# Performance work log

Measured on AMD Instinct MI355X. Metric: run time of the kernel, lower is better.

Reference implementation:

```python
import jax, jax.numpy as jnp
import numpy as np

B, T, D, H = 2, 2048, 2048, 16
DH = D // H

def setup_inputs() -> dict:
    key = jax.random.key(0)
    k1, k2, k3 = jax.random.split(key, 3)
    x = jax.random.normal(k1, (B, T, D), dtype=jnp.float32)
    w_qkv = jax.random.normal(k2, (D, 3 * D), dtype=jnp.float32) * (1.0 / np.sqrt(D))
    w_o = jax.random.normal(k3, (D, D), dtype=jnp.float32) * (1.0 / np.sqrt(D))
    return {"x": x, "w_qkv": w_qkv, "w_o": w_o}

def reference(x, w_qkv, w_o):
    b, t, d = x.shape
    qkv = (x @ w_qkv).reshape(b, t, 3, H, DH)
    q, k, v = qkv[:, :, 0], qkv[:, :, 1], qkv[:, :, 2]  # [b,t,h,dh]
    scale = 1.0 / np.sqrt(DH).astype(np.float32)
    # scores: [b,h,t,t]
    scores = jnp.einsum('bqhd,bkhd->bhqk', q, k) * scale
    causal = jnp.tril(jnp.ones((t, t), dtype=bool))
    scores = jnp.where(causal[None, None], scores, -jnp.inf)
    attn = jax.nn.softmax(scores, axis=-1)
    out = jnp.einsum('bhqk,bkhd->bqhd', attn, v).reshape(b, t, d)
    return out @ w_o
```

## Files before the change

kernel.cpp:

```cpp
#include <hip/hip_runtime.h>
#include <hip/hip_bf16.h>

#define B_   2
#define T_   2048
#define D_   2048
#define H_   16
#define DH_  128
#define TD3_ 6144

typedef __attribute__((ext_vector_type(8))) short   short8;
typedef __attribute__((ext_vector_type(8))) unsigned short ushort8v;
typedef __attribute__((ext_vector_type(4))) float   f32x4;
typedef __attribute__((ext_vector_type(4))) float   f4v;
typedef __attribute__((ext_vector_type(4))) unsigned short u16x4;

static __device__ __forceinline__ unsigned short f2bf(float f) {
  unsigned int u = __builtin_bit_cast(unsigned int, f);
  u += 0x7FFFu + ((u >> 16) & 1u);
  return (unsigned short)(u >> 16);
}
static __device__ __forceinline__ float bf2f(unsigned short u) {
  return __builtin_bit_cast(float, (unsigned int)u << 16);
}

static __device__ __forceinline__ void gload_lds16(const unsigned short* g, unsigned short* l) {
  __builtin_amdgcn_global_load_lds((const __attribute__((address_space(1))) void*)g,
                                   (__attribute__((address_space(3))) void*)l, 16, 0, 0);
}

__global__ __launch_bounds__(256) void convert_f32_bf16(const float* __restrict__ X,
                                                        unsigned short* __restrict__ Y, int n4) {
  for (int i = blockIdx.x * blockDim.x + threadIdx.x; i < n4; i += gridDim.x * blockDim.x) {
    f4v v = ((const f4v*)X)[i];
    u16x4 o;
    o[0] = f2bf(v[0]); o[1] = f2bf(v[1]); o[2] = f2bf(v[2]); o[3] = f2bf(v[3]);
    ((u16x4*)Y)[i] = o;
  }
}

__global__ __launch_bounds__(256) void transpose_f32_bf16(const float* __restrict__ W,
                                                          unsigned short* __restrict__ WT,
                                                          int K, int N) {
  __shared__ float tile[32][33];
  int n0 = blockIdx.x * 32, k0 = blockIdx.y * 32;
  int tx = threadIdx.x & 31, ty = threadIdx.x >> 5;
#pragma unroll
  for (int r = 0; r < 4; r++)
    tile[ty + 8 * r][tx] = W[(size_t)(k0 + ty + 8 * r) * N + n0 + tx];
  __syncthreads();
#pragma unroll
  for (int r = 0; r < 4; r++)
    WT[(size_t)(n0 + ty + 8 * r) * K + k0 + tx] = f2bf(tile[tx][ty + 8 * r]);
}

__global__ __launch_bounds__(256) void vtr_kernel(const unsigned short* __restrict__ qkv,
                                                  unsigned short* __restrict__ vtg) {
  __shared__ unsigned short tile[64][68];
  const int t0 = blockIdx.x * 64;
  const int h = blockIdx.y >> 1, dh0 = (blockIdx.y & 1) * 64;
  const int b = blockIdx.z;
  const int tid = threadIdx.x;
  const unsigned short* src = qkv + (size_t)b * T_ * TD3_ + 2 * D_ + h * DH_ + dh0;
  {
    const int r = tid >> 3, cc = (tid & 7) * 8;
#pragma unroll
    for (int k = 0; k < 2; k++) {
      ushort8v v = *(const ushort8v*)(src + (size_t)(t0 + k * 32 + r) * TD3_ + cc);
      *(ushort8v*)&tile[k * 32 + r][cc] = v;
    }
  }
  __syncthreads();
  unsigned short* dst = vtg + ((size_t)(b * H_ + h) * DH_ + dh0) * T_ + t0;
  {
    const int d = tid >> 3, tc = (tid & 7) * 8;
#pragma unroll
    for (int k = 0; k < 2; k++) {
      ushort8v v;
#pragma unroll
      for (int j = 0; j < 8; j++) v[j] = tile[tc + j][k * 32 + d];
      *(ushort8v*)(dst + (size_t)(k * 32 + d) * T_ + tc) = v;
    }
  }
}

template <int OUTBF>
__global__ __launch_bounds__(512, 1) void gemm256(const unsigned short* __restrict__ A,
                                                  const unsigned short* __restrict__ BT,
                                                  void* __restrict__ C, int M, int N, int K) {
  __shared__ unsigned short lA[2][2][128 * 64];
  __shared__ unsigned short lB[2][2][128 * 64];

  const int tid = threadIdx.x;
  const int nwg = gridDim.x;
  const int swz = ((int)blockIdx.x & 7) * (nwg >> 3) + ((int)blockIdx.x >> 3);
  const int nbx = N >> 8;
  const int m0 = (swz / nbx) * 256, n0 = (swz % nbx) * 256;
  const int l = tid & 63, lr = l & 15, lg = l >> 4;
  const int wid = tid >> 6, wm = wid >> 2, wn = wid & 3;
  const int bh = wn >> 1, br0 = (wn & 1) * 64;
  const int nk = K >> 6;

  f32x4 acc[8][4] = {};

  auto stageA = [&](int buf, int h, int kt) {
#pragma unroll
    for (int q = 0; q < 2; q++) {
      const int n = q * 512 + tid;
      const int row = n >> 3, ch = n & 7;
      gload_lds16(A + (size_t)(m0 + h * 128 + row) * K + kt * 64 + ((ch ^ (row & 7)) << 3),
                  &lA[buf][h][n * 8]);
    }
  };
  auto stageB = [&](int buf, int h, int kt) {
#pragma unroll
    for (int q = 0; q < 2; q++) {
      const int n = q * 512 + tid;
      const int row = n >> 3, ch = n & 7;
      gload_lds16(BT + (size_t)(n0 + h * 128 + row) * K + kt * 64 + ((ch ^ (row & 7)) << 3),
                  &lB[buf][h][n * 8]);
    }
  };

  stageB(0, 0, 0); stageA(0, 0, 0); stageB(0, 1, 0); stageA(0, 1, 0);
  if (nk > 1) {
    stageB(1, 0, 1); stageA(1, 0, 1);
    asm volatile("s_waitcnt vmcnt(4)" ::: "memory");
  } else {
    asm volatile("s_waitcnt vmcnt(0)" ::: "memory");
  }
  __builtin_amdgcn_s_barrier();

  short8 a[4][2], b0[2][2], b1[2][2];
  for (int kt = 0; kt < nk; kt++) {
    const int buf = kt & 1;

#pragma unroll
    for (int mi = 0; mi < 4; mi++)
#pragma unroll
      for (int kk = 0; kk < 2; kk++) {
        const int row = mi * 16 + lr;
        a[mi][kk] = *(const short8*)&lA[buf][wm][row * 64 + (((kk * 4 + lg) ^ (lr & 7)) << 3)];
      }
#pragma unroll
    for (int ni = 0; ni < 2; ni++)
#pragma unroll
      for (int kk = 0; kk < 2; kk++) {
        const int row = br0 + ni * 16 + lr;
        b0[ni][kk] = *(const short8*)&lB[buf][bh][row * 64 + (((kk * 4 + lg) ^ (lr & 7)) << 3)];
      }
    if (kt + 1 < nk) stageB(buf ^ 1, 1, kt + 1);
    __builtin_amdgcn_s_barrier();
    __builtin_amdgcn_s_setprio(1);
#pragma unroll
    for (int mi = 0; mi < 4; mi++)
#pragma unroll
      for (int ni = 0; ni < 2; ni++)
#pragma unroll
        for (int kk = 0; kk < 2; kk++)
          acc[mi][ni] = __builtin_amdgcn_mfma_f32_16x16x32_bf16(a[mi][kk], b0[ni][kk], acc[mi][ni], 0, 0, 0);
    __builtin_amdgcn_s_setprio(0);
    __builtin_amdgcn_s_barrier();

#pragma unroll
    for (int ni = 0; ni < 2; ni++)
#pragma unroll
      for (int kk = 0; kk < 2; kk++) {
        const int row = br0 + (2 + ni) * 16 + lr;
        b1[ni][kk] = *(const short8*)&lB[buf][bh][row * 64 + (((kk * 4 + lg) ^ (lr & 7)) << 3)];
      }
    if (kt + 1 < nk) stageA(buf ^ 1, 1, kt + 1);
    __builtin_amdgcn_s_barrier();
    __builtin_amdgcn_s_setprio(1);
#pragma unroll
    for (int mi = 0; mi < 4; mi++)
#pragma unroll
      for (int ni = 0; ni < 2; ni++)
#pragma unroll
        for (int kk = 0; kk < 2; kk++)
          acc[mi][2 + ni] = __builtin_amdgcn_mfma_f32_16x16x32_bf16(a[mi][kk], b1[ni][kk], acc[mi][2 + ni], 0, 0, 0);
    __builtin_amdgcn_s_setprio(0);
    __builtin_amdgcn_s_barrier();

#pragma unroll
    for (int mi = 0; mi < 4; mi++)
#pragma unroll
      for (int kk = 0; kk < 2; kk++) {
        const int row = (4 + mi) * 16 + lr;
        a[mi][kk] = *(const short8*)&lA[buf][wm][row * 64 + (((kk * 4 + lg) ^ (lr & 7)) << 3)];
      }
    if (kt + 2 < nk) stageB(buf, 0, kt + 2);
    __builtin_amdgcn_s_barrier();
    __builtin_amdgcn_s_setprio(1);
#pragma unroll
    for (int mi = 0; mi < 4; mi++)
#pragma unroll
      for (int ni = 0; ni < 2; ni++)
#pragma unroll
        for (int kk = 0; kk < 2; kk++)
          acc[4 + mi][2 + ni] = __builtin_amdgcn_mfma_f32_16x16x32_bf16(a[mi][kk], b1[ni][kk], acc[4 + mi][2 + ni], 0, 0, 0);
    __builtin_amdgcn_s_setprio(0);
    __builtin_amdgcn_s_barrier();

    if (kt + 2 < nk) stageA(buf, 0, kt + 2);
    __builtin_amdgcn_s_barrier();
    __builtin_amdgcn_s_setprio(1);
#pragma unroll
    for (int mi = 0; mi < 4; mi++)
#pragma unroll
      for (int ni = 0; ni < 2; ni++)
#pragma unroll
        for (int kk = 0; kk < 2; kk++)
          acc[4 + mi][ni] = __builtin_amdgcn_mfma_f32_16x16x32_bf16(a[mi][kk], b0[ni][kk], acc[4 + mi][ni], 0, 0, 0);
    __builtin_amdgcn_s_setprio(0);
    if (kt + 2 < nk) asm volatile("s_waitcnt vmcnt(4)" ::: "memory");
    else             asm volatile("s_waitcnt vmcnt(0)" ::: "memory");
    __builtin_amdgcn_s_barrier();
  }

#pragma unroll
  for (int mi = 0; mi < 8; mi++)
#pragma unroll
    for (int ni = 0; ni < 4; ni++)
#pragma unroll
      for (int i = 0; i < 4; i++) {
        const int row = m0 + wm * 128 + mi * 16 + lg * 4 + i;
        const int col = n0 + wn * 64 + ni * 16 + lr;
        if (OUTBF) ((unsigned short*)C)[(size_t)row * N + col] = f2bf(acc[mi][ni][i]);
        else       ((float*)C)[(size_t)row * N + col] = acc[mi][ni][i];
      }
}

__global__ __launch_bounds__(256, 2) void attn_fa(const unsigned short* __restrict__ qkv,
                                                  const unsigned short* __restrict__ vtg,
                                                  unsigned short* __restrict__ out) {
  const int x = blockIdx.x, h = blockIdx.y, b = blockIdx.z;
  const int qtl = b ? x : (T_ / 128 - 1 - x);
  const int q0 = qtl * 128;
  const int tid = threadIdx.x, w = tid >> 6, l = tid & 63, lr = l & 15, lg = l >> 4;

  const unsigned short* Qb = qkv + (size_t)b * T_ * TD3_ + h * DH_;
  const unsigned short* Kb = Qb + D_;
  const unsigned short* Vt = vtg + ((size_t)b * H_ + h) * DH_ * T_;

  __shared__ unsigned short klds[2][64 * 128];
  __shared__ unsigned short vt[2][128 * 64];
  __shared__ unsigned short plds[4][32 * 64];

  const float scale = 0.08838834764831845f;

  short8 qf[2][4];
#pragma unroll
  for (int mi = 0; mi < 2; mi++) {
    const unsigned short* qrow = Qb + (size_t)(q0 + w * 32 + mi * 16 + lr) * TD3_;
#pragma unroll
    for (int ks = 0; ks < 4; ks++) {
      ushort8v qv = *(const ushort8v*)(qrow + ks * 32 + lg * 8);
      short8 qs;
#pragma unroll
      for (int j = 0; j < 8; j++) qs[j] = (short)f2bf(bf2f(qv[j]) * scale);
      qf[mi][ks] = qs;
    }
  }

  f32x4 oacc[2][8] = {};
  float mrun[2][4], lsum[2][4];
#pragma unroll
  for (int mi = 0; mi < 2; mi++)
#pragma unroll
    for (int i = 0; i < 4; i++) { mrun[mi][i] = -__builtin_inff(); lsum[mi][i] = 0.f; }

  auto STAGE = [&](int buf, int kv0) {
#pragma unroll
    for (int it = 0; it < 4; it++) {
      const int n = it * 256 + tid;
      { const int kv = n >> 4, ch = n & 15;
        gload_lds16(Kb + (size_t)(kv0 + kv) * TD3_ + ((ch ^ (kv & 7)) << 3),
                    &klds[buf][n * 8]); }
      { const int dh = n >> 3, ch = n & 7;
        gload_lds16(Vt + (size_t)dh * T_ + kv0 + ((ch ^ (dh & 7)) << 3),
                    &vt[buf][n * 8]); }
    }
  };

  const int nt = 2 * qtl + 2;
  STAGE(0, 0);
  __syncthreads();

  for (int t = 0; t < nt; t++) {
    const int buf = t & 1;
    if (t + 1 < nt) STAGE(buf ^ 1, (t + 1) * 64);

    const int kv0 = t * 64;
    const bool active = (kv0 <= q0 + w * 32 + 31);
    if (active) {
      f32x4 s[2][4] = {};
      __builtin_amdgcn_s_setprio(1);
#pragma unroll
      for (int nf = 0; nf < 4; nf++) {
        const int kv = nf * 16 + lr;
#pragma unroll
        for (int ks = 0; ks < 4; ks++) {
          short8 kf = *(const short8*)&klds[buf][kv * 128 + (((ks * 4 + lg) ^ (lr & 7)) << 3)];
#pragma unroll
          for (int mi = 0; mi < 2; mi++)
            s[mi][nf] = __builtin_amdgcn_mfma_f32_16x16x32_bf16(qf[mi][ks], kf, s[mi][nf], 0, 0, 0);
        }
      }
      __builtin_amdgcn_s_setprio(0);

      const bool needmask = (kv0 + 63 > q0 + w * 32);
      float pmax[2][4];
#pragma unroll
      for (int mi = 0; mi < 2; mi++)
#pragma unroll
        for (int i = 0; i < 4; i++) pmax[mi][i] = -__builtin_inff();
#pragma unroll
      for (int mi = 0; mi < 2; mi++)
#pragma unroll
        for (int nf = 0; nf < 4; nf++)
#pragma unroll
          for (int i = 0; i < 4; i++) {
            float xv = s[mi][nf][i];
            if (needmask) {
              const int qr = w * 32 + mi * 16 + lg * 4 + i;
              const int kc = nf * 16 + lr;
              if (kv0 + kc > q0 + qr) xv = -__builtin_inff();
            }
            s[mi][nf][i] = xv;
            pmax[mi][i] = fmaxf(pmax[mi][i], xv);
          }
#pragma unroll
      for (int m = 1; m < 16; m <<= 1)
#pragma unroll
        for (int mi = 0; mi < 2; mi++)
#pragma unroll
          for (int i = 0; i < 4; i++) pmax[mi][i] = fmaxf(pmax[mi][i], __shfl_xor(pmax[mi][i], m));

      float alpha[2][4], rsum[2][4];
#pragma unroll
      for (int mi = 0; mi < 2; mi++)
#pragma unroll
        for (int i = 0; i < 4; i++) {
          const float mn = fmaxf(mrun[mi][i], pmax[mi][i]);
          alpha[mi][i] = __expf(mrun[mi][i] - mn);
          mrun[mi][i] = mn;
          rsum[mi][i] = 0.f;
        }
#pragma unroll
      for (int mi = 0; mi < 2; mi++)
#pragma unroll
        for (int nf = 0; nf < 4; nf++)
#pragma unroll
          for (int i = 0; i < 4; i++) {
            const float p = __expf(s[mi][nf][i] - mrun[mi][i]);
            rsum[mi][i] += p;
            const int prow = mi * 16 + lg * 4 + i;
            plds[w][prow * 64 + ((nf * 16 + lr) ^ ((prow & 7) << 3))] = f2bf(p);
          }
#pragma unroll
      for (int m = 1; m < 16; m <<= 1)
#pragma unroll
        for (int mi = 0; mi < 2; mi++)
#pragma unroll
          for (int i = 0; i < 4; i++) rsum[mi][i] += __shfl_xor(rsum[mi][i], m);
#pragma unroll
      for (int mi = 0; mi < 2; mi++)
#pragma unroll
        for (int i = 0; i < 4; i++) lsum[mi][i] = lsum[mi][i] * alpha[mi][i] + rsum[mi][i];
#pragma unroll
      for (int mi = 0; mi < 2; mi++)
#pragma unroll
        for (int nf = 0; nf < 8; nf++)
#pragma unroll
          for (int i = 0; i < 4; i++) oacc[mi][nf][i] *= alpha[mi][i];

      __builtin_amdgcn_s_setprio(1);
#pragma unroll
      for (int kk = 0; kk < 2; kk++) {
        short8 pa[2];
#pragma unroll
        for (int mi = 0; mi < 2; mi++) {
          const int prow = mi * 16 + lr;
          pa[mi] = *(const short8*)&plds[w][prow * 64 + (((kk * 32 + lg * 8)) ^ ((prow & 7) << 3))];
        }
#pragma unroll
        for (int nf = 0; nf < 8; nf++) {
          const short8 vb = *(const short8*)&vt[buf][(nf * 16 + lr) * 64 + (((kk * 4 + lg) ^ (lr & 7)) << 3)];
#pragma unroll
          for (int mi = 0; mi < 2; mi++)
            oacc[mi][nf] = __builtin_amdgcn_mfma_f32_16x16x32_bf16(pa[mi], vb, oacc[mi][nf], 0, 0, 0);
        }
      }
      __builtin_amdgcn_s_setprio(0);
    }
    __syncthreads();
  }

  float rinv[2][4];
#pragma unroll
  for (int mi = 0; mi < 2; mi++)
#pragma unroll
    for (int i = 0; i < 4; i++) rinv[mi][i] = 1.f / lsum[mi][i];
#pragma unroll
  for (int mi = 0; mi < 2; mi++) {
    unsigned short* orow = out + ((size_t)b * T_ + q0 + w * 32 + mi * 16 + lg * 4) * D_ + h * DH_;
#pragma unroll
    for (int nf = 0; nf < 8; nf++)
#pragma unroll
      for (int i = 0; i < 4; i++)
        orow[(size_t)i * D_ + nf * 16 + lr] = f2bf(oacc[mi][nf][i] * rinv[mi][i]);
  }
}

extern "C" void kernel_launch(void* const* d_in, const int* in_sizes, int n_in,
                              void* d_out, int out_size, void* d_ws, size_t ws_size,
                              hipStream_t stream) {
  const float* x    = (const float*)d_in[0];
  const float* wqkv = (const float*)d_in[1];
  const float* wo   = (const float*)d_in[2];
  float* out = (float*)d_out;

  char* ws = (char*)d_ws;
  unsigned short* xb    = (unsigned short*)(ws);
  unsigned short* wqkvt = (unsigned short*)(ws + 16777216);
  unsigned short* vtg   = (unsigned short*)(ws + 16777216);
  unsigned short* wot   = (unsigned short*)(ws + 41943040);
  unsigned short* qkv   = (unsigned short*)(ws + 50331648);
  unsigned short* attn  = xb;

  convert_f32_bf16<<<2048, 256, 0, stream>>>(x, xb, B_ * T_ * D_ / 4);
  transpose_f32_bf16<<<dim3(TD3_ / 32, D_ / 32), 256, 0, stream>>>(wqkv, wqkvt, D_, TD3_);
  transpose_f32_bf16<<<dim3(D_ / 32, D_ / 32), 256, 0, stream>>>(wo, wot, D_, D_);

  gemm256<1><<<dim3((TD3_ / 256) * ((B_ * T_) / 256)), 512, 0, stream>>>(xb, wqkvt, qkv,
                                                                         B_ * T_, TD3_, D_);
  vtr_kernel<<<dim3(T_ / 64, H_ * 2, B_), 256, 0, stream>>>(qkv, vtg);
  attn_fa<<<dim3(T_ / 128, H_, B_), 256, 0, stream>>>(qkv, vtg, attn);
  gemm256<0><<<dim3((D_ / 256) * ((B_ * T_) / 256)), 512, 0, stream>>>(attn, wot, out,
                                                                       B_ * T_, D_, D_);
}
```

Measured before the change: 311.9 us.

## Add 128x256-tile output projection GEMM and XCD-aware tile mapping

Replaces the templated GEMM with a bf16-only QKV GEMM whose block-to-tile mapping assigns contiguous N column ranges per XCD (bid&7), so each XCD's L2 reuses the same weight columns. Adds a separate output-projection kernel with 128x256 tiles, which doubles the workgroup count for the 4096x2048 GEMM (128 to 256 blocks) and fills more CUs. The new kernel uses a simpler double buffer that waits vmcnt(0) every iteration, giving less load/compute overlap than the original pipeline.

```diff
diff --git a/kernel.cpp b/kernel.cpp
--- a/kernel.cpp
+++ b/kernel.cpp
@@ -83,18 +83,20 @@
   }
 }
 
-template <int OUTBF>
 __global__ __launch_bounds__(512, 1) void gemm256(const unsigned short* __restrict__ A,
                                                   const unsigned short* __restrict__ BT,
-                                                  void* __restrict__ C, int M, int N, int K) {
+                                                  unsigned short* __restrict__ C,
+                                                  int M, int N, int K) {
   __shared__ unsigned short lA[2][2][128 * 64];
   __shared__ unsigned short lB[2][2][128 * 64];
 
   const int tid = threadIdx.x;
-  const int nwg = gridDim.x;
-  const int swz = ((int)blockIdx.x & 7) * (nwg >> 3) + ((int)blockIdx.x >> 3);
+  const int bid = (int)blockIdx.x;
   const int nbx = N >> 8;
-  const int m0 = (swz / nbx) * 256, n0 = (swz % nbx) * 256;
+  const int npx = nbx >> 3;
+  const int xcd = bid & 7, idx = bid >> 3;
+  const int n0 = (xcd * npx + idx % npx) * 256;
+  const int m0 = (idx / npx) * 256;
   const int l = tid & 63, lr = l & 15, lg = l >> 4;
   const int wid = tid >> 6, wm = wid >> 2, wn = wid & 3;
   const int bh = wn >> 1, br0 = (wn & 1) * 64;
@@ -225,8 +227,112 @@
       for (int i = 0; i < 4; i++) {
         const int row = m0 + wm * 128 + mi * 16 + lg * 4 + i;
         const int col = n0 + wn * 64 + ni * 16 + lr;
-        if (OUTBF) ((unsigned short*)C)[(size_t)row * N + col] = f2bf(acc[mi][ni][i]);
-        else       ((float*)C)[(size_t)row * N + col] = acc[mi][ni][i];
+        C[(size_t)row * N + col] = f2bf(acc[mi][ni][i]);
+      }
+}
+
+__global__ __launch_bounds__(512, 1) void gemm_op(const unsigned short* __restrict__ A,
+                                                  const unsigned short* __restrict__ BT,
+                                                  float* __restrict__ C,
+                                                  int M, int N, int K) {
+  __shared__ unsigned short lA[2][128 * 64];
+  __shared__ unsigned short lB[2][2][128 * 64];
+
+  const int tid = threadIdx.x;
+  const int bid = (int)blockIdx.x;
+  const int xcd = bid & 7, idx = bid >> 3;
+  const int n0 = xcd * 256, m0 = idx * 128;
+  const int l = tid & 63, lr = l & 15, lg = l >> 4;
+  const int wid = tid >> 6, wm = wid >> 2, wn = wid & 3;
+  const int bh = wn >> 1, br0 = (wn & 1) * 64;
+  const int nk = K >> 6;
+
+  f32x4 acc[4][4] = {};
+
+  auto stageA = [&](int buf, int kt) {
+#pragma unroll
+    for (int q = 0; q < 2; q++) {
+      const int n = q * 512 + tid;
+      const int row = n >> 3, ch = n & 7;
+      gload_lds16(A + (size_t)(m0 + row) * K + kt * 64 + ((ch ^ (row & 7)) << 3),
+                  &lA[buf][n * 8]);
+    }
+  };
+  auto stageB = [&](int buf, int h, int kt) {
+#pragma unroll
+    for (int q = 0; q < 2; q++) {
+      const int n = q * 512 + tid;
+      const int row = n >> 3, ch = n & 7;
+      gload_lds16(BT + (size_t)(n0 + h * 128 + row) * K + kt * 64 + ((ch ^ (row & 7)) << 3),
+                  &lB[buf][h][n * 8]);
+    }
+  };
+
+  stageB(0, 0, 0); stageB(0, 1, 0); stageA(0, 0);
+  asm volatile("s_waitcnt vmcnt(0)" ::: "memory");
+  __builtin_amdgcn_s_barrier();
+
+  short8 a[4][2], b0[2][2], b1[2][2];
+  for (int kt = 0; kt < nk; kt++) {
+    const int buf = kt & 1;
+
+    if (kt + 1 < nk) { stageB(buf ^ 1, 0, kt + 1); stageB(buf ^ 1, 1, kt + 1); stageA(buf ^ 1, kt + 1); }
+#pragma unroll
+    for (int mi = 0; mi < 4; mi++)
+#pragma unroll
+      for (int kk = 0; kk < 2; kk++) {
+        const int row = wm * 64 + mi * 16 + lr;
+        a[mi][kk] = *(const short8*)&lA[buf][row * 64 + (((kk * 4 + lg) ^ (lr & 7)) << 3)];
+      }
+#pragma unroll
+    for (int ni = 0; ni < 2; ni++)
+#pragma unroll
+      for (int kk = 0; kk < 2; kk++) {
+        const int row = br0 + ni * 16 + lr;
+        b0[ni][kk] = *(const short8*)&lB[buf][bh][row * 64 + (((kk * 4 + lg) ^ (lr & 7)) << 3)];
+      }
+    __builtin_amdgcn_s_barrier();
+    __builtin_amdgcn_s_setprio(1);
+#pragma unroll
+    for (int mi = 0; mi < 4; mi++)
+#pragma unroll
+      for (int ni = 0; ni < 2; ni++)
+#pragma unroll
+        for (int kk = 0; kk < 2; kk++)
+          acc[mi][ni] = __builtin_amdgcn_mfma_f32_16x16x32_bf16(a[mi][kk], b0[ni][kk], acc[mi][ni], 0, 0, 0);
+    __builtin_amdgcn_s_setprio(0);
+    __builtin_amdgcn_s_barrier();
+
+#pragma unroll
+    for (int ni = 0; ni < 2; ni++)
+#pragma unroll
+      for (int kk = 0; kk < 2; kk++) {
+        const int row = br0 + (2 + ni) * 16 + lr;
+        b1[ni][kk] = *(const short8*)&lB[buf][bh][row * 64 + (((kk * 4 + lg) ^ (lr & 7)) << 3)];
+      }
+    __builtin_amdgcn_s_barrier();
+    __builtin_amdgcn_s_setprio(1);
+#pragma unroll
+    for (int mi = 0; mi < 4; mi++)
+#pragma unroll
+      for (int ni = 0; ni < 2; ni++)
+#pragma unroll
+        for (int kk = 0; kk < 2; kk++)
+          acc[mi][2 + ni] = __builtin_amdgcn_mfma_f32_16x16x32_bf16(a[mi][kk], b1[ni][kk], acc[mi][2 + ni], 0, 0, 0);
+    __builtin_amdgcn_s_setprio(0);
+    asm volatile("s_waitcnt vmcnt(0)" ::: "memory");
+    __builtin_amdgcn_s_barrier();
+  }
+
+#pragma unroll
+  for (int mi = 0; mi < 4; mi++)
+#pragma unroll
+    for (int ni = 0; ni < 4; ni++)
+#pragma unroll
+      for (int i = 0; i < 4; i++) {
+        const int row = m0 + wm * 64 + mi * 16 + lg * 4 + i;
+        const int col = n0 + wn * 64 + ni * 16 + lr;
+        C[(size_t)row * N + col] = acc[mi][ni][i];
       }
 }
 
@@ -432,10 +538,10 @@
   transpose_f32_bf16<<<dim3(TD3_ / 32, D_ / 32), 256, 0, stream>>>(wqkv, wqkvt, D_, TD3_);
   transpose_f32_bf16<<<dim3(D_ / 32, D_ / 32), 256, 0, stream>>>(wo, wot, D_, D_);
 
-  gemm256<1><<<dim3((TD3_ / 256) * ((B_ * T_) / 256)), 512, 0, stream>>>(xb, wqkvt, qkv,
-                                                                         B_ * T_, TD3_, D_);
+  gemm256<<<dim3((TD3_ / 256) * ((B_ * T_) / 256)), 512, 0, stream>>>(xb, wqkvt, qkv,
+                                                                      B_ * T_, TD3_, D_);
   vtr_kernel<<<dim3(T_ / 64, H_ * 2, B_), 256, 0, stream>>>(qkv, vtg);
   attn_fa<<<dim3(T_ / 128, H_, B_), 256, 0, stream>>>(qkv, vtg, attn);
-  gemm256<0><<<dim3((D_ / 256) * ((B_ * T_) / 256)), 512, 0, stream>>>(attn, wot, out,
-                                                                       B_ * T_, D_, D_);
-}
+  gemm_op<<<dim3((D_ / 256) * ((B_ * T_) / 128)), 512, 0, stream>>>(attn, wot, out,
+                                                                    B_ * T_, D_, D_);
+}
```

After: 307.4 us. About the same (-1.4%).
